# Optimization experiments

Hardware: AMD Instinct MI355X
Metric: run time of the kernel (lower is better)

The kernel has to match this reference:

```python
import jax, jax.numpy as jnp
import numpy as np
import math

D_MODEL = 1024
ED = 2048       # d_inner = expand * d_model
R = 64          # dt_rank = ceil(d_model/16)
N = 16          # d_state
K = 4           # d_conv
DT_MIN, DT_MAX, DT_FLOOR = 0.001, 0.1, 0.0001


def setup_inputs() -> dict:
    key = jax.random.key(0)
    ks = jax.random.split(key, 8)
    x = jax.random.normal(ks[0], (1, 2048, D_MODEL), dtype=jnp.float32)
    in_proj_w = jax.random.normal(ks[1], (2 * ED, D_MODEL), dtype=jnp.float32) * (D_MODEL ** -0.5)
    conv_w = jax.random.normal(ks[2], (ED, 1, K), dtype=jnp.float32) * (K ** -0.5)
    conv_b = jnp.zeros((ED,), dtype=jnp.float32)
    x_proj_w = jax.random.normal(ks[3], (R + 2 * N, ED), dtype=jnp.float32) * (ED ** -0.5)
    std = R ** -0.5
    dt_proj_w = jax.random.uniform(ks[4], (ED, R), dtype=jnp.float32, minval=-std, maxval=std)
    dt = jnp.exp(jax.random.uniform(ks[5], (ED,), dtype=jnp.float32)
                 * (math.log(DT_MAX) - math.log(DT_MIN)) + math.log(DT_MIN))
    dt = jnp.clip(dt, DT_FLOOR, None)
    dt_proj_b = dt + jnp.log(-jnp.expm1(-dt))  # inverse softplus init
    A_log = jnp.log(jnp.tile(jnp.arange(1, N + 1, dtype=jnp.float32), (ED, 1)))  # [ED, N]
    D = jnp.ones((ED,), dtype=jnp.float32)
    out_proj_w = jax.random.normal(ks[6], (D_MODEL, ED), dtype=jnp.float32) * (ED ** -0.5)
    return {"x": x, "in_proj_w": in_proj_w, "conv_w": conv_w, "conv_b": conv_b,
            "x_proj_w": x_proj_w, "dt_proj_w": dt_proj_w, "dt_proj_b": dt_proj_b,
            "A_log": A_log, "D": D, "out_proj_w": out_proj_w}


def _causal_dwconv(xr, conv_w, conv_b):
    # xr: [B, L, ED]; depthwise causal conv, left-pad K-1 (equiv to pad K-1 both sides then slice [:L])
    x_ncl = jnp.transpose(xr, (0, 2, 1))
    y = jax.lax.conv_general_dilated(x_ncl, conv_w, window_strides=(1,),
                                     padding=[(K - 1, 0)], feature_group_count=ED)
    return jnp.transpose(y, (0, 2, 1)) + conv_b


def _mamba_fwd(x, in_proj_w, conv_w, conv_b, x_proj_w, dt_proj_w, dt_proj_b, A_log, D, out_proj_w):
    xz = jnp.einsum('bld,ed->ble', x, in_proj_w)          # [B, L, 2*ED]
    xr, z = jnp.split(xz, 2, axis=-1)
    xr = jax.nn.silu(_causal_dwconv(xr, conv_w, conv_b))  # [B, L, ED]
    A = -jnp.exp(A_log)                                    # [ED, N]
    dbc = jnp.einsum('ble,fe->blf', xr, x_proj_w)          # [B, L, R+2N]
    delta_r, Bm, Cm = jnp.split(dbc, [R, R + N], axis=-1)
    delta = jax.nn.softplus(jnp.einsum('blr,er->ble', delta_r, dt_proj_w) + dt_proj_b)  # [B, L, ED]
    dA = jnp.exp(delta[..., None] * A)                     # [B, L, ED, N]
    BX = delta[..., None] * Bm[:, :, None, :] * xr[..., None]  # [B, L, ED, N]
    # linear recurrence h_t = dA_t * h_{t-1} + BX_t via associative scan over L
    def combine(c1, c2):
        a1, x1 = c1
        a2, x2 = c2
        return a1 * a2, a2 * x1 + x2
    _, hs = jax.lax.associative_scan(combine, (dA, BX), axis=1)  # [B, L, ED, N]
    y = jnp.einsum('blen,bln->ble', hs, Cm) + D * xr
    return jnp.einsum('ble,de->bld', y * jax.nn.silu(z), out_proj_w)


def reference(x, in_proj_w, conv_w, conv_b, x_proj_w, dt_proj_w, dt_proj_b, A_log, D, out_proj_w):
    return _mamba_fwd(x, in_proj_w, conv_w, conv_b, x_proj_w, dt_proj_w, dt_proj_b, A_log, D, out_proj_w)
```

## Files before the change

kernel.cpp:

```cpp
#include <hip/hip_runtime.h>
#include <math.h>

#define LSEQ 2048
#define DM   1024
#define EDIM 2048
#define RNK  64
#define NS   16
#define DBCW 96
#define LC   32
#define NCH  (LSEQ / LC)
#define NSEG 8
#define SPLITK2 16
#define SPLITK4 4

typedef __attribute__((ext_vector_type(4))) float f32x4;
typedef __attribute__((ext_vector_type(8))) __bf16 bf16x8;

__device__ __forceinline__ ushort f2bf(float f) {
    unsigned u = __float_as_uint(f);
    unsigned r = (u + 0x7fffu + ((u >> 16) & 1u)) >> 16;
    return (ushort)r;
}
__device__ __forceinline__ float bf2f(ushort u) {
    return __uint_as_float(((unsigned)u) << 16);
}

#define R0 2097152L
#define R1 (R0 + 4194304L)
#define R2 (R1 + 2097152L)
#define R3 (R2 + 196608L)
#define R4 (R3 + 131072L)
#define R5 (R4 + 32768L)

__global__ __launch_bounds__(256) void prep_all(
    const float* __restrict__ x, const float* __restrict__ w1,
    const float* __restrict__ w4, const float* __restrict__ xpw,
    const float* __restrict__ w3,
    ushort* __restrict__ xbf, ushort* __restrict__ w1bf,
    ushort* __restrict__ w4bf, ushort* __restrict__ xpw_pad,
    ushort* __restrict__ w3bf)
{
    long idx4 = ((long)blockIdx.x * 256 + threadIdx.x) * 4;
    if (idx4 >= R5) return;
    if (idx4 >= R4) {
        long rel = idx4 - R4;
        float* p = (float*)(xpw_pad + 196608);
        *reinterpret_cast<float4*>(&p[rel]) = make_float4(0.f, 0.f, 0.f, 0.f);
        return;
    }
    const float* src; ushort* dst; long rel;
    if (idx4 < R0)      { src = x;   dst = xbf;     rel = idx4; }
    else if (idx4 < R1) { src = w1;  dst = w1bf;    rel = idx4 - R0; }
    else if (idx4 < R2) { src = w4;  dst = w4bf;    rel = idx4 - R1; }
    else if (idx4 < R3) { src = xpw; dst = xpw_pad; rel = idx4 - R2; }
    else                { src = w3;  dst = w3bf;    rel = idx4 - R3; }
    float4 v = *reinterpret_cast<const float4*>(&src[rel]);
    ushort4 o = make_ushort4(f2bf(v.x), f2bf(v.y), f2bf(v.z), f2bf(v.w));
    *reinterpret_cast<ushort4*>(&dst[rel]) = o;
}

template<int EPI>
__global__ __launch_bounds__(256) void gemm_nt_bf16(
    const ushort* __restrict__ A, int lda,
    const ushort* __restrict__ B, int ldb,
    float* __restrict__ C0, float* __restrict__ C1, int csplit, int ldc,
    long cplane, int klen, int grid_n, int blocks_per_k,
    const float* __restrict__ bias)
{
    __shared__ ushort As[128 * 32];
    __shared__ ushort Bs[128 * 32];
    const int tid = threadIdx.x;
    const int wave = tid >> 6;
    const int lane = tid & 63;
    const int kch = blockIdx.x / blocks_per_k;
    const int rem = blockIdx.x % blocks_per_k;
    const int bm = (rem / grid_n) * 128;
    const int bn = (rem % grid_n) * 128;
    const int wm = (wave & 1) * 64;
    const int wn = (wave >> 1) * 64;
    const int koff = kch * klen;
    C0 += (long)kch * cplane;

    f32x4 acc[4][4] = {};

    const int offT = tid * 16;
    const char* Ab = (const char*)A;
    const char* Bb = (const char*)B;
    char* AsB = (char*)As;
    char* BsB = (char*)Bs;

    for (int k0 = 0; k0 < klen; k0 += 32) {
        __syncthreads();
        #pragma unroll
        for (int r = 0; r < 2; ++r) {
            int off = r * 4096 + offT;
            int row = off >> 6;
            int kb = off & 63;
            __builtin_amdgcn_global_load_lds(
                (const __attribute__((address_space(1))) void*)
                    (Ab + ((long)(bm + row) * lda + koff + k0) * 2 + kb),
                (__attribute__((address_space(3))) void*)
                    (AsB + r * 4096 + wave * 1024), 16, 0, 0);
            __builtin_amdgcn_global_load_lds(
                (const __attribute__((address_space(1))) void*)
                    (Bb + ((long)(bn + row) * ldb + koff + k0) * 2 + kb),
                (__attribute__((address_space(3))) void*)
                    (BsB + r * 4096 + wave * 1024), 16, 0, 0);
        }
        __syncthreads();

        bf16x8 af[4], bfr[4];
        #pragma unroll
        for (int i = 0; i < 4; ++i) {
            int ar = wm + i * 16 + (lane & 15);
            af[i]  = *reinterpret_cast<const bf16x8*>(AsB + ar * 64 + (lane >> 4) * 16);
            int br = wn + i * 16 + (lane & 15);
            bfr[i] = *reinterpret_cast<const bf16x8*>(BsB + br * 64 + (lane >> 4) * 16);
        }
        #pragma unroll
        for (int i = 0; i < 4; ++i)
            #pragma unroll
            for (int j = 0; j < 4; ++j)
                acc[i][j] = __builtin_amdgcn_mfma_f32_16x16x32_bf16(
                    af[i], bfr[j], acc[i][j], 0, 0, 0);
    }

    #pragma unroll
    for (int i = 0; i < 4; ++i) {
        int row0 = bm + wm + i * 16 + (lane >> 4) * 4;
        #pragma unroll
        for (int j = 0; j < 4; ++j) {
            int col = bn + wn + j * 16 + (lane & 15);
            float* Cp;
            int cc;
            if (col < csplit) { Cp = C0; cc = col; }
            else              { Cp = C1; cc = col - csplit; }
            float bv = (EPI == 1) ? bias[col] : 0.f;
            #pragma unroll
            for (int q = 0; q < 4; ++q) {
                float v = acc[i][j][q];
                if (EPI == 1) {
                    v += bv;
                    v = fmaxf(v, 0.f) + log1pf(__expf(-fabsf(v)));
                }
                Cp[(long)(row0 + q) * ldc + cc] = v;
            }
        }
    }
}

__global__ __launch_bounds__(256) void g4_reduce(
    const float* __restrict__ Gp, float* __restrict__ out)
{
    long i4 = ((long)blockIdx.x * 256 + threadIdx.x) * 4;
    float4 a = *reinterpret_cast<const float4*>(&Gp[i4]);
    float4 b = *reinterpret_cast<const float4*>(&Gp[2097152 + i4]);
    float4 c = *reinterpret_cast<const float4*>(&Gp[4194304 + i4]);
    float4 d = *reinterpret_cast<const float4*>(&Gp[6291456 + i4]);
    float4 o = make_float4(a.x + b.x + c.x + d.x, a.y + b.y + c.y + d.y,
                           a.z + b.z + c.z + d.z, a.w + b.w + c.w + d.w);
    *reinterpret_cast<float4*>(&out[i4]) = o;
}

__global__ __launch_bounds__(256) void gemm2_reduce(
    const float* __restrict__ Pb, float* __restrict__ dbc,
    ushort* __restrict__ dtr)
{
    int idx = blockIdx.x * 256 + threadIdx.x;
    float s = 0.f;
    #pragma unroll
    for (int c = 0; c < SPLITK2; ++c) s += Pb[(long)c * LSEQ * DBCW + idx];
    dbc[idx] = s;
    int r = idx / DBCW;
    int c = idx - r * DBCW;
    if (c < RNK) dtr[r * RNK + c] = f2bf(s);
}

__global__ __launch_bounds__(256) void conv_silu(
    const float* __restrict__ xr, const float* __restrict__ w,
    const float* __restrict__ b, ushort* __restrict__ xrc)
{
    int idx = blockIdx.x * 256 + threadIdx.x;
    int l = idx >> 9;
    int e4 = (idx & 511) << 2;
    float4 zero = make_float4(0.f, 0.f, 0.f, 0.f);
    float4 r0 = (l >= 3) ? *reinterpret_cast<const float4*>(&xr[(long)(l - 3) * EDIM + e4]) : zero;
    float4 r1 = (l >= 2) ? *reinterpret_cast<const float4*>(&xr[(long)(l - 2) * EDIM + e4]) : zero;
    float4 r2 = (l >= 1) ? *reinterpret_cast<const float4*>(&xr[(long)(l - 1) * EDIM + e4]) : zero;
    float4 r3 = *reinterpret_cast<const float4*>(&xr[(long)l * EDIM + e4]);
    float4 bb = *reinterpret_cast<const float4*>(&b[e4]);
    float rr0[4] = {r0.x, r0.y, r0.z, r0.w};
    float rr1[4] = {r1.x, r1.y, r1.z, r1.w};
    float rr2[4] = {r2.x, r2.y, r2.z, r2.w};
    float rr3[4] = {r3.x, r3.y, r3.z, r3.w};
    float bbv[4] = {bb.x, bb.y, bb.z, bb.w};
    ushort o[4];
    #pragma unroll
    for (int j = 0; j < 4; ++j) {
        float4 wj = *reinterpret_cast<const float4*>(&w[(e4 + j) * 4]);
        float acc = bbv[j];
        acc = fmaf(wj.x, rr0[j], acc);
        acc = fmaf(wj.y, rr1[j], acc);
        acc = fmaf(wj.z, rr2[j], acc);
        acc = fmaf(wj.w, rr3[j], acc);
        o[j] = f2bf(acc / (1.f + __expf(-acc)));
    }
    *reinterpret_cast<ushort4*>(&xrc[(long)l * EDIM + e4]) =
        make_ushort4(o[0], o[1], o[2], o[3]);
}

__global__ __launch_bounds__(256) void scan_phaseA(
    const float* __restrict__ delta, const ushort* __restrict__ xr,
    const float* __restrict__ dbc, const float* __restrict__ A_log,
    float* __restrict__ P, float* __restrict__ Hf)
{
    int g = blockIdx.x * 256 + threadIdx.x;
    int e = g & (EDIM - 1);
    int c = g >> 11;
    float Aa[NS], h[NS], Pp[NS];
    #pragma unroll
    for (int n = 0; n < NS; ++n) {
        Aa[n] = -__expf(A_log[e * NS + n]);
        h[n] = 0.f;
        Pp[n] = 1.f;
    }
    int t0 = c * LC;
    for (int t = t0; t < t0 + LC; ++t) {
        float d  = delta[(long)t * EDIM + e];
        float xv = bf2f(xr[(long)t * EDIM + e]);
        const float* bm = dbc + (long)t * DBCW + RNK;
        float dx = d * xv;
        #pragma unroll
        for (int n = 0; n < NS; ++n) {
            float a = __expf(d * Aa[n]);
            h[n] = fmaf(a, h[n], dx * bm[n]);
            Pp[n] *= a;
        }
    }
    #pragma unroll
    for (int n = 0; n < NS; ++n) {
        P [(long)(c * NS + n) * EDIM + e] = Pp[n];
        Hf[(long)(c * NS + n) * EDIM + e] = h[n];
    }
}

__global__ __launch_bounds__(256) void scan_phaseB1(
    float* __restrict__ P, float* __restrict__ Hf,
    float* __restrict__ Sp, float* __restrict__ Sf)
{
    int gid = blockIdx.x * 256 + threadIdx.x;
    int e = gid & (EDIM - 1);
    int n = (gid >> 11) & (NS - 1);
    int g = gid >> 15;
    float h = 0.f, pp = 1.f;
    for (int c = g * NSEG; c < g * NSEG + NSEG; ++c) {
        long idx = (long)(c * NS + n) * EDIM + e;
        float p = P[idx];
        float f = Hf[idx];
        Hf[idx] = h;
        P[idx] = pp;
        h = fmaf(p, h, f);
        pp *= p;
    }
    long si = (long)(g * NS + n) * EDIM + e;
    Sp[si] = pp;
    Sf[si] = h;
}

__global__ __launch_bounds__(256) void scan_phaseB2(
    const float* __restrict__ Sp, float* __restrict__ Sf)
{
    int gid = blockIdx.x * 256 + threadIdx.x;
    int e = gid & (EDIM - 1);
    int n = gid >> 11;
    float h = 0.f;
    for (int g = 0; g < NSEG; ++g) {
        long idx = (long)(g * NS + n) * EDIM + e;
        float p = Sp[idx];
        float f = Sf[idx];
        Sf[idx] = h;
        h = fmaf(p, h, f);
    }
}

__global__ __launch_bounds__(256) void scan_phaseC(
    const float* __restrict__ delta, const ushort* __restrict__ xr,
    const float* __restrict__ dbc, const float* __restrict__ A_log,
    const float* __restrict__ P, const float* __restrict__ Hf,
    const float* __restrict__ Sf, const float* __restrict__ Dp,
    const float* __restrict__ z, ushort* __restrict__ ubf)
{
    int gid = blockIdx.x * 256 + threadIdx.x;
    int e = gid & (EDIM - 1);
    int c = gid >> 11;
    int g = c >> 3;
    float Aa[NS], h[NS];
    #pragma unroll
    for (int n = 0; n < NS; ++n) {
        Aa[n] = -__expf(A_log[e * NS + n]);
        long ci = (long)(c * NS + n) * EDIM + e;
        long si = (long)(g * NS + n) * EDIM + e;
        h[n] = fmaf(P[ci], Sf[si], Hf[ci]);
    }
    float dD = Dp[e];
    int t0 = c * LC;
    for (int t = t0; t < t0 + LC; ++t) {
        float d  = delta[(long)t * EDIM + e];
        float xv = bf2f(xr[(long)t * EDIM + e]);
        const float* bm = dbc + (long)t * DBCW + RNK;
        const float* cm = dbc + (long)t * DBCW + RNK + NS;
        float dx = d * xv;
        float y = 0.f;
        #pragma unroll
        for (int n = 0; n < NS; ++n) {
            float a = __expf(d * Aa[n]);
            h[n] = fmaf(a, h[n], dx * bm[n]);
            y = fmaf(h[n], cm[n], y);
        }
        y = fmaf(dD, xv, y);
        float zv = z[(long)t * EDIM + e];
        float sz = zv / (1.f + __expf(-zv));
        ubf[(long)t * EDIM + e] = f2bf(y * sz);
    }
}

extern "C" void kernel_launch(void* const* d_in, const int* in_sizes, int n_in,
                              void* d_out, int out_size, void* d_ws, size_t ws_size,
                              hipStream_t stream) {
    const float* x         = (const float*)d_in[0];
    const float* in_proj_w = (const float*)d_in[1];
    const float* conv_w    = (const float*)d_in[2];
    const float* conv_b    = (const float*)d_in[3];
    const float* x_proj_w  = (const float*)d_in[4];
    const float* dt_proj_w = (const float*)d_in[5];
    const float* dt_proj_b = (const float*)d_in[6];
    const float* A_log     = (const float*)d_in[7];
    const float* Dp        = (const float*)d_in[8];
    const float* out_proj_w= (const float*)d_in[9];
    float* out = (float*)d_out;

    float* ws = (float*)d_ws;
    const long M1 = 1048576;
    ushort* xbf     = (ushort*)ws;
    ushort* w1bf    = (ushort*)(ws + 1 * M1);
    float*  Pb      = ws;
    ushort* ubf     = (ushort*)ws;
    float*  junk    = ws + 3 * M1;
    ushort* xpw_pad = (ushort*)(ws + 3 * M1 + M1 / 4);
    ushort* w4bf    = (ushort*)(ws + 3 * M1 + M1 / 2);
    float*  xr_f32  = ws + 4 * M1 + M1 / 2;
    float*  delta   = xr_f32;
    float*  z_f32   = ws + 8 * M1 + M1 / 2;
    float*  Gp      = ws + 4 * M1 + M1 / 2;
    ushort* xrcbf   = (ushort*)(ws + 12 * M1 + M1 / 2);
    float*  P       = ws + 14 * M1 + M1 / 2;
    float*  Hf      = ws + 16 * M1 + M1 / 2;
    float*  Sp      = ws + 18 * M1 + M1 / 2;
    float*  Sf      = ws + 18 * M1 + 3 * M1 / 4;
    float*  dbc     = ws + 19 * M1;
    ushort* w3bf    = (ushort*)(ws + 19 * M1 + 196608);
    ushort* dtr_bf  = (ushort*)(ws + 19 * M1 + 196608 + 65536);

    dim3 blk(256);

    prep_all<<<(R5 / 4 + 255) / 256, blk, 0, stream>>>(
        x, in_proj_w, out_proj_w, x_proj_w, dt_proj_w,
        xbf, w1bf, w4bf, xpw_pad, w3bf);

    gemm_nt_bf16<0><<<512, blk, 0, stream>>>(
        xbf, DM, w1bf, DM, xr_f32, z_f32, EDIM, EDIM, 0, DM, 32, 512, nullptr);

    conv_silu<<<(LSEQ * EDIM) / 1024, blk, 0, stream>>>(xr_f32, conv_w, conv_b, xrcbf);

    gemm_nt_bf16<0><<<SPLITK2 * 16, blk, 0, stream>>>(
        xrcbf, EDIM, xpw_pad, EDIM, Pb, junk, DBCW, DBCW,
        (long)LSEQ * DBCW, EDIM / SPLITK2, 1, 16, nullptr);
    gemm2_reduce<<<(LSEQ * DBCW) / 256, blk, 0, stream>>>(Pb, dbc, dtr_bf);

    gemm_nt_bf16<1><<<256, blk, 0, stream>>>(
        dtr_bf, RNK, w3bf, RNK, delta, junk, 1 << 30, EDIM, 0, RNK, 16, 256,
        dt_proj_b);

    scan_phaseA<<<(NCH * EDIM) / 256, blk, 0, stream>>>(
        delta, xrcbf, dbc, A_log, P, Hf);
    scan_phaseB1<<<(EDIM * NS * NSEG) / 256, blk, 0, stream>>>(P, Hf, Sp, Sf);
    scan_phaseB2<<<(EDIM * NS) / 256, blk, 0, stream>>>(Sp, Sf);
    scan_phaseC<<<(NCH * EDIM) / 256, blk, 0, stream>>>(
        delta, xrcbf, dbc, A_log, P, Hf, Sf, Dp, z_f32, ubf);

    gemm_nt_bf16<0><<<SPLITK4 * 128, blk, 0, stream>>>(
        ubf, EDIM, w4bf, EDIM, Gp, junk, 1 << 30, DM,
        (long)LSEQ * DM, EDIM / SPLITK4, 8, 128, nullptr);
    g4_reduce<<<(LSEQ * DM) / 1024, blk, 0, stream>>>(Gp, out);
}
```

Baseline: 182.5 us.

## Fuse dt_proj GEMM and softplus into scan phases A and C

Removes the separate delta GEMM (dt_proj with softplus epilogue) and instead recomputes delta per timestep inside both scan_phaseA and scan_phaseC. Each block stages the 32x64 dt_rank chunk in shared memory and each thread keeps its 64 dt_proj weights in registers for a scalar dot product. This avoids writing and reading back the 16 MB fp32 delta tensor and saves a launch. In exchange it computes the rank-64 projection twice with scalar FMAs instead of MFMA and raises register pressure in the scan kernels.

```diff
diff --git a/kernel.cpp b/kernel.cpp
--- a/kernel.cpp
+++ b/kernel.cpp
@@ -59,13 +59,11 @@
     *reinterpret_cast<ushort4*>(&dst[rel]) = o;
 }
 
-template<int EPI>
 __global__ __launch_bounds__(256) void gemm_nt_bf16(
     const ushort* __restrict__ A, int lda,
     const ushort* __restrict__ B, int ldb,
     float* __restrict__ C0, float* __restrict__ C1, int csplit, int ldc,
-    long cplane, int klen, int grid_n, int blocks_per_k,
-    const float* __restrict__ bias)
+    long cplane, int klen, int grid_n, int blocks_per_k)
 {
     __shared__ ushort As[128 * 32];
     __shared__ ushort Bs[128 * 32];
@@ -135,16 +133,9 @@
             int cc;
             if (col < csplit) { Cp = C0; cc = col; }
             else              { Cp = C1; cc = col - csplit; }
-            float bv = (EPI == 1) ? bias[col] : 0.f;
             #pragma unroll
-            for (int q = 0; q < 4; ++q) {
-                float v = acc[i][j][q];
-                if (EPI == 1) {
-                    v += bv;
-                    v = fmaxf(v, 0.f) + log1pf(__expf(-fabsf(v)));
-                }
-                Cp[(long)(row0 + q) * ldc + cc] = v;
-            }
+            for (int q = 0; q < 4; ++q)
+                Cp[(long)(row0 + q) * ldc + cc] = acc[i][j][q];
         }
     }
 }
@@ -209,14 +200,44 @@
         make_ushort4(o[0], o[1], o[2], o[3]);
 }
 
+__device__ __forceinline__ float delta_dot(
+    const ushort* __restrict__ dls, int tt, const bf16x8* w3r, float be)
+{
+    float sd = be;
+    #pragma unroll
+    for (int j = 0; j < 8; ++j) {
+        bf16x8 dr = *reinterpret_cast<const bf16x8*>(&dls[tt * 64 + j * 8]);
+        #pragma unroll
+        for (int k = 0; k < 8; ++k)
+            sd = fmaf((float)dr[k], (float)w3r[j][k], sd);
+    }
+    return fmaxf(sd, 0.f) + log1pf(__expf(-fabsf(sd)));
+}
+
 __global__ __launch_bounds__(256) void scan_phaseA(
-    const float* __restrict__ delta, const ushort* __restrict__ xr,
-    const float* __restrict__ dbc, const float* __restrict__ A_log,
+    const ushort* __restrict__ dtr, const ushort* __restrict__ w3,
+    const float* __restrict__ dtb,
+    const ushort* __restrict__ xr, const float* __restrict__ dbc,
+    const float* __restrict__ A_log,
     float* __restrict__ P, float* __restrict__ Hf)
 {
+    __shared__ ushort dls[LC * RNK];
     int g = blockIdx.x * 256 + threadIdx.x;
     int e = g & (EDIM - 1);
     int c = g >> 11;
+    int t0 = c * LC;
+    {
+        int i = threadIdx.x;
+        *reinterpret_cast<uint4*>(&dls[(i >> 3) * RNK + (i & 7) * 8]) =
+            *reinterpret_cast<const uint4*>(&dtr[(long)(t0 + (i >> 3)) * RNK + (i & 7) * 8]);
+    }
+    bf16x8 w3r[8];
+    #pragma unroll
+    for (int j = 0; j < 8; ++j)
+        w3r[j] = *reinterpret_cast<const bf16x8*>(&w3[(long)e * RNK + j * 8]);
+    float be = dtb[e];
+    __syncthreads();
+
     float Aa[NS], h[NS], Pp[NS];
     #pragma unroll
     for (int n = 0; n < NS; ++n) {
@@ -224,9 +245,9 @@
         h[n] = 0.f;
         Pp[n] = 1.f;
     }
-    int t0 = c * LC;
-    for (int t = t0; t < t0 + LC; ++t) {
-        float d  = delta[(long)t * EDIM + e];
+    for (int tt = 0; tt < LC; ++tt) {
+        int t = t0 + tt;
+        float d  = delta_dot(dls, tt, w3r, be);
         float xv = bf2f(xr[(long)t * EDIM + e]);
         const float* bm = dbc + (long)t * DBCW + RNK;
         float dx = d * xv;
@@ -284,16 +305,32 @@
 }
 
 __global__ __launch_bounds__(256) void scan_phaseC(
-    const float* __restrict__ delta, const ushort* __restrict__ xr,
-    const float* __restrict__ dbc, const float* __restrict__ A_log,
+    const ushort* __restrict__ dtr, const ushort* __restrict__ w3,
+    const float* __restrict__ dtb,
+    const ushort* __restrict__ xr, const float* __restrict__ dbc,
+    const float* __restrict__ A_log,
     const float* __restrict__ P, const float* __restrict__ Hf,
     const float* __restrict__ Sf, const float* __restrict__ Dp,
     const float* __restrict__ z, ushort* __restrict__ ubf)
 {
+    __shared__ ushort dls[LC * RNK];
     int gid = blockIdx.x * 256 + threadIdx.x;
     int e = gid & (EDIM - 1);
     int c = gid >> 11;
     int g = c >> 3;
+    int t0 = c * LC;
+    {
+        int i = threadIdx.x;
+        *reinterpret_cast<uint4*>(&dls[(i >> 3) * RNK + (i & 7) * 8]) =
+            *reinterpret_cast<const uint4*>(&dtr[(long)(t0 + (i >> 3)) * RNK + (i & 7) * 8]);
+    }
+    bf16x8 w3r[8];
+    #pragma unroll
+    for (int j = 0; j < 8; ++j)
+        w3r[j] = *reinterpret_cast<const bf16x8*>(&w3[(long)e * RNK + j * 8]);
+    float be = dtb[e];
+    __syncthreads();
+
     float Aa[NS], h[NS];
     #pragma unroll
     for (int n = 0; n < NS; ++n) {
@@ -303,9 +340,9 @@
         h[n] = fmaf(P[ci], Sf[si], Hf[ci]);
     }
     float dD = Dp[e];
-    int t0 = c * LC;
-    for (int t = t0; t < t0 + LC; ++t) {
-        float d  = delta[(long)t * EDIM + e];
+    for (int tt = 0; tt < LC; ++tt) {
+        int t = t0 + tt;
+        float d  = delta_dot(dls, tt, w3r, be);
         float xv = bf2f(xr[(long)t * EDIM + e]);
         const float* bm = dbc + (long)t * DBCW + RNK;
         const float* cm = dbc + (long)t * DBCW + RNK + NS;
@@ -349,7 +386,6 @@
     ushort* xpw_pad = (ushort*)(ws + 3 * M1 + M1 / 4);
     ushort* w4bf    = (ushort*)(ws + 3 * M1 + M1 / 2);
     float*  xr_f32  = ws + 4 * M1 + M1 / 2;
-    float*  delta   = xr_f32;
     float*  z_f32   = ws + 8 * M1 + M1 / 2;
     float*  Gp      = ws + 4 * M1 + M1 / 2;
     ushort* xrcbf   = (ushort*)(ws + 12 * M1 + M1 / 2);
@@ -367,29 +403,25 @@
         x, in_proj_w, out_proj_w, x_proj_w, dt_proj_w,
         xbf, w1bf, w4bf, xpw_pad, w3bf);
 
-    gemm_nt_bf16<0><<<512, blk, 0, stream>>>(
-        xbf, DM, w1bf, DM, xr_f32, z_f32, EDIM, EDIM, 0, DM, 32, 512, nullptr);
+    gemm_nt_bf16<<<512, blk, 0, stream>>>(
+        xbf, DM, w1bf, DM, xr_f32, z_f32, EDIM, EDIM, 0, DM, 32, 512);
 
     conv_silu<<<(LSEQ * EDIM) / 1024, blk, 0, stream>>>(xr_f32, conv_w, conv_b, xrcbf);
 
-    gemm_nt_bf16<0><<<SPLITK2 * 16, blk, 0, stream>>>(
+    gemm_nt_bf16<<<SPLITK2 * 16, blk, 0, stream>>>(
         xrcbf, EDIM, xpw_pad, EDIM, Pb, junk, DBCW, DBCW,
-        (long)LSEQ * DBCW, EDIM / SPLITK2, 1, 16, nullptr);
+        (long)LSEQ * DBCW, EDIM / SPLITK2, 1, 16);
     gemm2_reduce<<<(LSEQ * DBCW) / 256, blk, 0, stream>>>(Pb, dbc, dtr_bf);
 
-    gemm_nt_bf16<1><<<256, blk, 0, stream>>>(
-        dtr_bf, RNK, w3bf, RNK, delta, junk, 1 << 30, EDIM, 0, RNK, 16, 256,
-        dt_proj_b);
-
     scan_phaseA<<<(NCH * EDIM) / 256, blk, 0, stream>>>(
-        delta, xrcbf, dbc, A_log, P, Hf);
+        dtr_bf, w3bf, dt_proj_b, xrcbf, dbc, A_log, P, Hf);
     scan_phaseB1<<<(EDIM * NS * NSEG) / 256, blk, 0, stream>>>(P, Hf, Sp, Sf);
     scan_phaseB2<<<(EDIM * NS) / 256, blk, 0, stream>>>(Sp, Sf);
     scan_phaseC<<<(NCH * EDIM) / 256, blk, 0, stream>>>(
-        delta, xrcbf, dbc, A_log, P, Hf, Sf, Dp, z_f32, ubf);
-
-    gemm_nt_bf16<0><<<SPLITK4 * 128, blk, 0, stream>>>(
+        dtr_bf, w3bf, dt_proj_b, xrcbf, dbc, A_log, P, Hf, Sf, Dp, z_f32, ubf);
+
+    gemm_nt_bf16<<<SPLITK4 * 128, blk, 0, stream>>>(
         ubf, EDIM, w4bf, EDIM, Gp, junk, 1 << 30, DM,
-        (long)LSEQ * DM, EDIM / SPLITK4, 8, 128, nullptr);
+        (long)LSEQ * DM, EDIM / SPLITK4, 8, 128);
     g4_reduce<<<(LSEQ * DM) / 1024, blk, 0, stream>>>(Gp, out);
 }
```

New measurement: 229.0 us. 1.25x slower.
